# Kernel tuning notes

Hardware: AMD Instinct MI355X
Metric: run time of the kernel (lower is better)

The kernel has to match this reference:

```python
import jax, jax.numpy as jnp
import numpy as np

H, HK, HD = 6, 2, 128  # n_heads, n_kv_heads, head_dim (from AcousticTransformerArgs defaults)


def setup_inputs() -> dict:
    key = jax.random.key(0)
    k1, k2, k3, k4, k5 = jax.random.split(key, 5)
    B, S, D = 2, 4096, 768
    s = 0.02
    return {
        "x": jax.random.normal(k1, (B, S, D), dtype=jnp.float32),
        "wq": jax.random.normal(k2, (H * HD, D), dtype=jnp.float32) * s,
        "wk": jax.random.normal(k3, (HK * HD, D), dtype=jnp.float32) * s,
        "wv": jax.random.normal(k4, (HK * HD, D), dtype=jnp.float32) * s,
        "wo": jax.random.normal(k5, (D, H * HD), dtype=jnp.float32) * s,
    }


def reference(x, wq, wk, wv, wo):
    B, S, D = x.shape
    rep = H // HK  # GQA repeat factor (3)
    scale = 1.0 / jnp.sqrt(jnp.asarray(HD, x.dtype))
    # projections (torch Linear: y = x @ W^T)
    q = (x @ wq.T).reshape(B, S, HK, rep, HD) * scale  # head h = g*rep + r
    k = (x @ wk.T).reshape(B, S, HK, HD)
    v = (x @ wv.T).reshape(B, S, HK, HD)
    # bidirectional (no mask) attention with GQA broadcast instead of physical repeat
    scores = jnp.einsum("bsgrd,btgd->bgrst", q, k)  # [B,HK,rep,S,S]
    attn = jax.nn.softmax(scores, axis=-1)
    out = jnp.einsum("bgrst,btgd->bsgrd", attn, v).reshape(B, S, H * HD)
    return out @ wo.T
```

## Files before the change

### kernel.cpp

```cpp
#include <hip/hip_runtime.h>
#include <hip/hip_bf16.h>
#include <type_traits>

using bf16 = __hip_bfloat16;
typedef __attribute__((ext_vector_type(8))) short bf16x8;
typedef __attribute__((ext_vector_type(4))) float floatx4;

static constexpr int Bb = 2, S = 4096, D = 768, H = 6, HK = 2, HD = 128, REP = 3;
static constexpr int M_ROWS = Bb * S;
static constexpr int NQKV = 1280;

__device__ __forceinline__ floatx4 mfma16(bf16x8 a, bf16x8 b, floatx4 c) {
  return __builtin_amdgcn_mfma_f32_16x16x32_bf16(a, b, c, 0, 0, 0);
}

__device__ __forceinline__ void gld_lds16(const bf16* g, bf16* l) {
  __builtin_amdgcn_global_load_lds(
      (const __attribute__((address_space(1))) unsigned int*)g,
      (__attribute__((address_space(3))) unsigned int*)l, 16, 0, 0);
}

#if defined(__has_builtin)
#if __has_builtin(__builtin_amdgcn_exp2f)
#define EXP2F(x) __builtin_amdgcn_exp2f(x)
#endif
#endif
#ifndef EXP2F
#define EXP2F(x) exp2f(x)
#endif

__device__ __forceinline__ unsigned pk2(float a, float b) {
  unsigned ua = __builtin_bit_cast(unsigned, a) + 0x8000u;
  unsigned ub = __builtin_bit_cast(unsigned, b) + 0x8000u;
#if defined(__has_builtin) && __has_builtin(__builtin_amdgcn_perm)
  return __builtin_amdgcn_perm(ub, ua, 0x07060302);
#else
  return (ua >> 16) | (ub & 0xffff0000u);
#endif
}

__device__ __forceinline__ void perm32swap(unsigned& a, unsigned& b) {
  asm volatile("v_permlane32_swap_b32 %0, %1" : "+v"(a), "+v"(b));
}
__device__ __forceinline__ void perm16swap(unsigned& a, unsigned& b) {
  asm volatile("v_permlane16_swap_b32 %0, %1" : "+v"(a), "+v"(b));
}

static constexpr size_t E_X  = (size_t)M_ROWS * D;
static constexpr size_t E_WQ = E_X + (size_t)H * HD * D;
static constexpr size_t E_WK = E_WQ + (size_t)HK * HD * D;
static constexpr size_t E_WV = E_WK + (size_t)HK * HD * D;
static constexpr size_t E_WO = E_WV + (size_t)D * H * HD;

__global__ __launch_bounds__(256) void cvt_all(const float* __restrict__ x,
                                               const float* __restrict__ wq,
                                               const float* __restrict__ wk,
                                               const float* __restrict__ wv,
                                               const float* __restrict__ wo,
                                               bf16* __restrict__ xb,
                                               bf16* __restrict__ wqkvb,
                                               bf16* __restrict__ wob, float qscale) {
  size_t i = ((size_t)blockIdx.x * 256 + threadIdx.x) * 4;
  const float* src;
  bf16* dst;
  float s = 1.f;
  size_t off;
  if (i < E_X)        { src = x;  dst = xb;                 off = i; }
  else if (i < E_WQ)  { src = wq; dst = wqkvb;              off = i - E_X; s = qscale; }
  else if (i < E_WK)  { src = wk; dst = wqkvb + 589824;     off = i - E_WQ; }
  else if (i < E_WV)  { src = wv; dst = wqkvb + 786432;     off = i - E_WK; }
  else                { src = wo; dst = wob;                off = i - E_WV; }
  float4 v = *(const float4*)(src + off);
  uint2 st;
  st.x = pk2(v.x * s, v.y * s);
  st.y = pk2(v.z * s, v.w * s);
  *(uint2*)(dst + off) = st;
}

template <typename OutT, bool VT_FUSE>
__global__ __launch_bounds__(256, 3) void gemm_bt(const bf16* __restrict__ A,
                                                  const bf16* __restrict__ W,
                                                  OutT* __restrict__ C,
                                                  bf16* __restrict__ Vt,
                                                  int M, int N, int K) {
  const int tid = threadIdx.x;
  const int wave = tid >> 6, lane = tid & 63;
  const int quad = lane >> 4, lq = lane & 15;
  const int m0 = blockIdx.x * 128, n0 = blockIdx.y * 128;
  const int wm = (wave & 1) * 64, wn = (wave >> 1) * 64;

  __shared__ __align__(16) bf16 As[128 * 64];
  __shared__ __align__(16) bf16 Ws[128 * 64];

  floatx4 acc[4][4] = {};

  const int srow = lane >> 3, sc = lane & 7;

  for (int k0 = 0; k0 < K; k0 += 64) {
#pragma unroll
    for (int i = 0; i < 4; ++i) {
      int ig = wave * 4 + i;
      int r = ig * 8 + srow;
      int c = sc ^ (r & 7);
      gld_lds16(&A[(size_t)(m0 + r) * K + k0 + c * 8], &As[ig * 512]);
      gld_lds16(&W[(size_t)(n0 + r) * K + k0 + c * 8], &Ws[ig * 512]);
    }
    __syncthreads();
#pragma unroll
    for (int kh = 0; kh < 2; ++kh) {
      bf16x8 af[4], wf[4];
#pragma unroll
      for (int i = 0; i < 4; ++i) {
        int ra = wm + i * 16 + lq, rw = wn + i * 16 + lq;
        af[i] = *(const bf16x8*)&As[ra * 64 + (((kh * 4 + quad) ^ (ra & 7)) * 8)];
        wf[i] = *(const bf16x8*)&Ws[rw * 64 + (((kh * 4 + quad) ^ (rw & 7)) * 8)];
      }
#pragma unroll
      for (int i = 0; i < 4; ++i)
#pragma unroll
        for (int j = 0; j < 4; ++j) acc[i][j] = mfma16(af[i], wf[j], acc[i][j]);
    }
    __syncthreads();
  }

  if (VT_FUSE && n0 >= 1024) {
    bf16* tb = (wave < 2 ? As : Ws) + (wave & 1) * 4096;
    char* tc = (char*)tb;
#pragma unroll
    for (int i = 0; i < 4; ++i)
#pragma unroll
      for (int j = 0; j < 4; ++j) {
        uint2 st;
        st.x = pk2(acc[i][j][0], acc[i][j][1]);
        st.y = pk2(acc[i][j][2], acc[i][j][3]);
        int col = j * 16 + lq;
        int cc = (i * 2 + (quad >> 1)) ^ (col & 7);
        *(uint2*)(tc + col * 128 + cc * 16 + (quad & 1) * 8) = st;
      }
    const int b = m0 >> 12;
    const int dd_off = lane >> 3, schunk = lane & 7;
    const int sbase = (m0 & 4095) + wm + schunk * 8;
#pragma unroll
    for (int e = 0; e < 8; ++e) {
      int cl = e * 8 + dd_off;
      int col = (n0 - 1024) + wn + cl;
      int gg = col >> 7, dd = col & 127;
      bf16x8 vv = *(const bf16x8*)(tc + cl * 128 + ((schunk ^ (cl & 7)) * 16));
      *(bf16x8*)&Vt[((size_t)(b * HK + gg) * HD + dd) * S + sbase] = vv;
    }
    return;
  }
#pragma unroll
  for (int i = 0; i < 4; ++i)
#pragma unroll
    for (int j = 0; j < 4; ++j)
#pragma unroll
      for (int r = 0; r < 4; ++r) {
        int row = m0 + wm + i * 16 + quad * 4 + r;
        int col = n0 + wn + j * 16 + lq;
        float v = acc[i][j][r];
        if constexpr (std::is_same_v<OutT, float>)
          C[(size_t)row * N + col] = v;
        else
          C[(size_t)row * N + col] = __float2bfloat16(v);
      }
}

__global__ __launch_bounds__(256, 3) void gemm_out(const bf16* __restrict__ A,
                                                   const bf16* __restrict__ W,
                                                   float* __restrict__ C,
                                                   int M, int N, int K) {
  const int tid = threadIdx.x;
  const int wave = tid >> 6, lane = tid & 63;
  const int quad = lane >> 4, lq = lane & 15;
  const int m0 = blockIdx.x * 128, n0 = blockIdx.y * 64;
  const int wm = (wave & 1) * 64, wn = (wave >> 1) * 32;

  __shared__ __align__(16) bf16 As[128 * 64];
  __shared__ __align__(16) bf16 Ws[64 * 64];

  floatx4 acc[4][2] = {};

  const int srow = lane >> 3, sc = lane & 7;

  for (int k0 = 0; k0 < K; k0 += 64) {
#pragma unroll
    for (int i = 0; i < 4; ++i) {
      int ig = wave * 4 + i;
      int r = ig * 8 + srow;
      int c = sc ^ (r & 7);
      gld_lds16(&A[(size_t)(m0 + r) * K + k0 + c * 8], &As[ig * 512]);
    }
#pragma unroll
    for (int i = 0; i < 2; ++i) {
      int ig = wave * 2 + i;
      int r = ig * 8 + srow;
      int c = sc ^ (r & 7);
      gld_lds16(&W[(size_t)(n0 + r) * K + k0 + c * 8], &Ws[ig * 512]);
    }
    __syncthreads();
#pragma unroll
    for (int kh = 0; kh < 2; ++kh) {
      bf16x8 af[4], wf[2];
#pragma unroll
      for (int i = 0; i < 4; ++i) {
        int ra = wm + i * 16 + lq;
        af[i] = *(const bf16x8*)&As[ra * 64 + (((kh * 4 + quad) ^ (ra & 7)) * 8)];
      }
#pragma unroll
      for (int j = 0; j < 2; ++j) {
        int rw = wn + j * 16 + lq;
        wf[j] = *(const bf16x8*)&Ws[rw * 64 + (((kh * 4 + quad) ^ (rw & 7)) * 8)];
      }
#pragma unroll
      for (int i = 0; i < 4; ++i)
#pragma unroll
        for (int j = 0; j < 2; ++j) acc[i][j] = mfma16(af[i], wf[j], acc[i][j]);
    }
    __syncthreads();
  }
#pragma unroll
  for (int i = 0; i < 4; ++i)
#pragma unroll
    for (int j = 0; j < 2; ++j)
#pragma unroll
      for (int r = 0; r < 4; ++r) {
        int row = m0 + wm + i * 16 + quad * 4 + r;
        int col = n0 + wn + j * 16 + lq;
        C[(size_t)row * N + col] = acc[i][j][r];
      }
}

__global__ __launch_bounds__(256, 2) void flash_attn(const bf16* __restrict__ QKV,
                                                     const bf16* __restrict__ Vt,
                                                     bf16* __restrict__ O) {
  const int bid = blockIdx.x;
  const int bg = (bid & 7) >> 1;
  const int b = bg >> 1, g = bg & 1;
  const int qt = ((bid >> 3) << 1) | (bid & 1);
  const int q0 = qt * 32;

  const int tid = threadIdx.x;
  const int w = tid >> 6, lane = tid & 63;
  const int half = w >> 1, wp = w & 1;
  const int quad = lane >> 4, lq = lane & 15;

  __shared__ __align__(16) char smem[81920];
  bf16* Ks = (bf16*)smem;
  bf16* Vs = (bf16*)(smem + 32768);

  const bf16* Kgh = QKV + (size_t)b * S * NQKV + H * HD + g * HD + (size_t)half * 2048 * NQKV;
  const bf16* Vgh = Vt + (size_t)(b * HK + g) * HD * S + half * 2048;

  auto stage = [&](int t0, int kbuf, int vbuf) {
    bf16* kd = Ks + (kbuf * 2 + half) * 4096;
    bf16* vd = Vs + (vbuf * 2 + half) * 4096;
#pragma unroll
    for (int i = 0; i < 4; ++i) {
      int ig = wp * 4 + i;
      int tl = ig * 4 + (lane >> 4);
      int c = (lane & 15) ^ (tl & 15);
      gld_lds16(Kgh + (size_t)(t0 + tl) * NQKV + c * 8, kd + ig * 512);
    }
#pragma unroll
    for (int i = 0; i < 4; ++i) {
      int ig = wp * 4 + i;
      int dl = ig * 16 + (lane >> 2);
      int c = (lane & 3) ^ ((dl >> 1) & 3);
      gld_lds16(Vgh + (size_t)dl * S + t0 + c * 8, vd + ig * 512);
    }
  };

  stage(0, 0, 0);

  const bf16* Qg = QKV + ((size_t)b * S + q0 + wp * 16 + lq) * NQKV + g * REP * HD;
  bf16x8 qf[3][4];
#pragma unroll
  for (int u = 0; u < 3; ++u)
#pragma unroll
    for (int kk = 0; kk < 4; ++kk)
      qf[u][kk] = *(const bf16x8*)(Qg + u * HD + kk * 32 + quad * 8);

  bf16x8 ones;
#pragma unroll
  for (int j = 0; j < 8; ++j) ones[j] = (short)0x3F80;

  floatx4 o[3][8] = {};
  floatx4 lacc[3] = {};
  bf16x8 pf_prev[3];
  const int sw = (lq >> 1) & 3;

#pragma unroll 2
  for (int it = 0; it < 64; ++it) {
    const int kcur = it & 1;
    __syncthreads();
    if (it + 1 < 64) stage((it + 1) * 32, kcur ^ 1, (it + 1) % 3);

    const bf16* ks = Ks + (kcur * 2 + half) * 4096;

    floatx4 sf[3][2] = {};
    __builtin_amdgcn_s_setprio(1);
#pragma unroll
    for (int tt = 0; tt < 2; ++tt)
#pragma unroll
      for (int kk = 0; kk < 4; ++kk) {
        int c = (kk * 4 + quad) ^ lq;
        bf16x8 kf = *(const bf16x8*)&ks[(tt * 16 + lq) * 128 + c * 8];
#pragma unroll
        for (int u = 0; u < 3; ++u) sf[u][tt] = mfma16(kf, qf[u][kk], sf[u][tt]);
      }

    if (it) {
      const bf16* vs = Vs + ((((it - 1) % 3) * 2) + half) * 4096;
#pragma unroll
      for (int u = 0; u < 3; ++u) lacc[u] = mfma16(ones, pf_prev[u], lacc[u]);
#pragma unroll
      for (int dd = 0; dd < 8; ++dd) {
        bf16x8 vf = *(const bf16x8*)&vs[(dd * 16 + lq) * 32 + ((quad ^ sw) * 8)];
#pragma unroll
        for (int u = 0; u < 3; ++u) o[u][dd] = mfma16(vf, pf_prev[u], o[u][dd]);
      }
    }
    __builtin_amdgcn_s_setprio(0);

#pragma unroll
    for (int u = 0; u < 3; ++u) {
      unsigned A0 = pk2(EXP2F(sf[u][0][0]), EXP2F(sf[u][0][1]));
      unsigned A1 = pk2(EXP2F(sf[u][0][2]), EXP2F(sf[u][0][3]));
      unsigned B0 = pk2(EXP2F(sf[u][1][0]), EXP2F(sf[u][1][1]));
      unsigned B1 = pk2(EXP2F(sf[u][1][2]), EXP2F(sf[u][1][3]));
      perm32swap(A0, B0);
      perm16swap(A0, B0);
      perm32swap(A1, B1);
      perm16swap(A1, B1);
      union { unsigned d[4]; bf16x8 v; } pu;
      pu.d[0] = A0; pu.d[1] = A1; pu.d[2] = B0; pu.d[3] = B1;
      pf_prev[u] = pu.v;
    }
  }

  {
    const bf16* vs = Vs + (0 * 2 + half) * 4096;
#pragma unroll
    for (int u = 0; u < 3; ++u) lacc[u] = mfma16(ones, pf_prev[u], lacc[u]);
#pragma unroll
    for (int dd = 0; dd < 8; ++dd) {
      bf16x8 vf = *(const bf16x8*)&vs[(dd * 16 + lq) * 32 + ((quad ^ sw) * 8)];
#pragma unroll
      for (int u = 0; u < 3; ++u) o[u][dd] = mfma16(vf, pf_prev[u], o[u][dd]);
    }
  }

  __syncthreads();
  floatx4* oscr = (floatx4*)smem;
  float* lscr = (float*)(smem + 49152);
  if (half == 1) {
#pragma unroll
    for (int u = 0; u < 3; ++u) {
#pragma unroll
      for (int dd = 0; dd < 8; ++dd)
        oscr[((wp * 3 + u) * 8 + dd) * 64 + lane] = o[u][dd];
      lscr[(wp * 3 + u) * 64 + lane] = lacc[u][0];
    }
  }
  __syncthreads();
  if (half == 0) {
    const size_t row = (size_t)b * S + q0 + wp * 16 + lq;
#pragma unroll
    for (int u = 0; u < 3; ++u) {
      float l = lacc[u][0] + lscr[(wp * 3 + u) * 64 + lane];
      float rinv = 1.0f / l;
#pragma unroll
      for (int dd = 0; dd < 8; ++dd) {
        floatx4 oc = o[u][dd] + oscr[((wp * 3 + u) * 8 + dd) * 64 + lane];
        uint2 st;
        st.x = pk2(oc[0] * rinv, oc[1] * rinv);
        st.y = pk2(oc[2] * rinv, oc[3] * rinv);
        int col = (g * REP + u) * HD + dd * 16 + quad * 4;
        *(uint2*)&O[row * (H * HD) + col] = st;
      }
    }
  }
}

static inline size_t al256(size_t x) { return (x + 255) & ~size_t(255); }

extern "C" void kernel_launch(void* const* d_in, const int* in_sizes, int n_in,
                              void* d_out, int out_size, void* d_ws, size_t ws_size,
                              hipStream_t stream) {
  const float* x  = (const float*)d_in[0];
  const float* wq = (const float*)d_in[1];
  const float* wk = (const float*)d_in[2];
  const float* wv = (const float*)d_in[3];
  const float* wo = (const float*)d_in[4];
  float* out = (float*)d_out;

  char* w = (char*)d_ws;
  size_t off = 0;
  auto carve = [&](size_t elems) {
    bf16* p = (bf16*)(w + off);
    off = al256(off + elems * sizeof(bf16));
    return p;
  };
  bf16* xb    = carve((size_t)M_ROWS * D);
  bf16* wqkvb = carve((size_t)NQKV * D);
  bf16* wob   = carve((size_t)D * (H * HD));
  bf16* QKVb  = carve((size_t)M_ROWS * NQKV);
  bf16* Vtb   = carve((size_t)M_ROWS * (HK * HD));
  bf16* Ab    = carve((size_t)M_ROWS * (H * HD));

  const float qscale = 0.1275174465f;

  cvt_all<<<(int)(E_WO / 1024), 256, 0, stream>>>(x, wq, wk, wv, wo, xb, wqkvb, wob, qscale);

  gemm_bt<bf16, true><<<dim3(M_ROWS / 128, NQKV / 128), 256, 0, stream>>>(
      xb, wqkvb, QKVb, Vtb, M_ROWS, NQKV, D);

  flash_attn<<<512, 256, 0, stream>>>(QKVb, Vtb, Ab);

  gemm_out<<<dim3(M_ROWS / 128, D / 64), 256, 0, stream>>>(
      Ab, wob, out, M_ROWS, D, H * HD);
}
```

Baseline: 220.9 us.

## Remove split-KV halves in flash attention; two waves scan full sequence

Flash attention blocks drop from four waves (two KV halves) to two waves that each iterate over the full key sequence. This removes the shared-memory cross-half reduction and its barriers, halves shared memory per block, and precomputes staging pointers incremented each step. In exchange, each block runs twice as many serial iterations with fewer waves, reducing latency hiding.

```diff
diff --git a/kernel.cpp b/kernel.cpp
--- a/kernel.cpp
+++ b/kernel.cpp
@@ -231,7 +231,7 @@
       }
 }
 
-__global__ __launch_bounds__(256, 2) void flash_attn(const bf16* __restrict__ QKV,
+__global__ __launch_bounds__(128, 2) void flash_attn(const bf16* __restrict__ QKV,
                                                      const bf16* __restrict__ Vt,
                                                      bf16* __restrict__ O) {
   const int bid = blockIdx.x;
@@ -241,37 +241,43 @@
   const int q0 = qt * 32;
 
   const int tid = threadIdx.x;
-  const int w = tid >> 6, lane = tid & 63;
-  const int half = w >> 1, wp = w & 1;
+  const int wp = tid >> 6, lane = tid & 63;
   const int quad = lane >> 4, lq = lane & 15;
 
-  __shared__ __align__(16) char smem[81920];
+  __shared__ __align__(16) char smem[40960];
   bf16* Ks = (bf16*)smem;
-  bf16* Vs = (bf16*)(smem + 32768);
-
-  const bf16* Kgh = QKV + (size_t)b * S * NQKV + H * HD + g * HD + (size_t)half * 2048 * NQKV;
-  const bf16* Vgh = Vt + (size_t)(b * HK + g) * HD * S + half * 2048;
-
-  auto stage = [&](int t0, int kbuf, int vbuf) {
-    bf16* kd = Ks + (kbuf * 2 + half) * 4096;
-    bf16* vd = Vs + (vbuf * 2 + half) * 4096;
-#pragma unroll
-    for (int i = 0; i < 4; ++i) {
-      int ig = wp * 4 + i;
-      int tl = ig * 4 + (lane >> 4);
-      int c = (lane & 15) ^ (tl & 15);
-      gld_lds16(Kgh + (size_t)(t0 + tl) * NQKV + c * 8, kd + ig * 512);
-    }
-#pragma unroll
-    for (int i = 0; i < 4; ++i) {
-      int ig = wp * 4 + i;
-      int dl = ig * 16 + (lane >> 2);
-      int c = (lane & 3) ^ ((dl >> 1) & 3);
-      gld_lds16(Vgh + (size_t)dl * S + t0 + c * 8, vd + ig * 512);
-    }
+  bf16* Vs = (bf16*)(smem + 16384);
+
+  const bf16* Kgh = QKV + (size_t)b * S * NQKV + H * HD + g * HD;
+  const bf16* Vgh = Vt + (size_t)(b * HK + g) * HD * S;
+
+  const bf16* kp[4];
+  const bf16* vp[4];
+#pragma unroll
+  for (int i = 0; i < 4; ++i) {
+    int tl = wp * 16 + i * 4 + (lane >> 4);
+    int c = (lane & 15) ^ (tl & 15);
+    kp[i] = Kgh + (size_t)tl * NQKV + c * 8;
+  }
+#pragma unroll
+  for (int i = 0; i < 4; ++i) {
+    int dl = wp * 64 + i * 16 + (lane >> 2);
+    int c = (lane & 3) ^ ((dl >> 1) & 3);
+    vp[i] = Vgh + (size_t)dl * S + c * 8;
+  }
+
+  auto stage = [&](int kbuf, int vbuf) {
+    bf16* kd = Ks + kbuf * 4096;
+    bf16* vd = Vs + vbuf * 4096;
+#pragma unroll
+    for (int i = 0; i < 4; ++i) gld_lds16(kp[i], kd + (wp * 4 + i) * 512);
+#pragma unroll
+    for (int i = 0; i < 4; ++i) gld_lds16(vp[i], vd + (wp * 4 + i) * 512);
+#pragma unroll
+    for (int i = 0; i < 4; ++i) { kp[i] += 32 * NQKV; vp[i] += 32; }
   };
 
-  stage(0, 0, 0);
+  stage(0, 0);
 
   const bf16* Qg = QKV + ((size_t)b * S + q0 + wp * 16 + lq) * NQKV + g * REP * HD;
   bf16x8 qf[3][4];
@@ -291,12 +297,11 @@
   const int sw = (lq >> 1) & 3;
 
 #pragma unroll 2
-  for (int it = 0; it < 64; ++it) {
-    const int kcur = it & 1;
+  for (int it = 0; it < 128; ++it) {
     __syncthreads();
-    if (it + 1 < 64) stage((it + 1) * 32, kcur ^ 1, (it + 1) % 3);
-
-    const bf16* ks = Ks + (kcur * 2 + half) * 4096;
+    if (it + 1 < 128) stage((it + 1) & 1, (it + 1) % 3);
+
+    const bf16* ks = Ks + (it & 1) * 4096;
 
     floatx4 sf[3][2] = {};
     __builtin_amdgcn_s_setprio(1);
@@ -311,7 +316,7 @@
       }
 
     if (it) {
-      const bf16* vs = Vs + ((((it - 1) % 3) * 2) + half) * 4096;
+      const bf16* vs = Vs + ((it - 1) % 3) * 4096;
 #pragma unroll
       for (int u = 0; u < 3; ++u) lacc[u] = mfma16(ones, pf_prev[u], lacc[u]);
 #pragma unroll
@@ -340,7 +345,7 @@
   }
 
   {
-    const bf16* vs = Vs + (0 * 2 + half) * 4096;
+    const bf16* vs = Vs + 1 * 4096;
 #pragma unroll
     for (int u = 0; u < 3; ++u) lacc[u] = mfma16(ones, pf_prev[u], lacc[u]);
 #pragma unroll
@@ -351,34 +356,17 @@
     }
   }
 
-  __syncthreads();
-  floatx4* oscr = (floatx4*)smem;
-  float* lscr = (float*)(smem + 49152);
-  if (half == 1) {
-#pragma unroll
-    for (int u = 0; u < 3; ++u) {
-#pragma unroll
-      for (int dd = 0; dd < 8; ++dd)
-        oscr[((wp * 3 + u) * 8 + dd) * 64 + lane] = o[u][dd];
-      lscr[(wp * 3 + u) * 64 + lane] = lacc[u][0];
-    }
-  }
-  __syncthreads();
-  if (half == 0) {
-    const size_t row = (size_t)b * S + q0 + wp * 16 + lq;
-#pragma unroll
-    for (int u = 0; u < 3; ++u) {
-      float l = lacc[u][0] + lscr[(wp * 3 + u) * 64 + lane];
-      float rinv = 1.0f / l;
-#pragma unroll
-      for (int dd = 0; dd < 8; ++dd) {
-        floatx4 oc = o[u][dd] + oscr[((wp * 3 + u) * 8 + dd) * 64 + lane];
-        uint2 st;
-        st.x = pk2(oc[0] * rinv, oc[1] * rinv);
-        st.y = pk2(oc[2] * rinv, oc[3] * rinv);
-        int col = (g * REP + u) * HD + dd * 16 + quad * 4;
-        *(uint2*)&O[row * (H * HD) + col] = st;
-      }
+  const size_t row = (size_t)b * S + q0 + wp * 16 + lq;
+#pragma unroll
+  for (int u = 0; u < 3; ++u) {
+    float rinv = 1.0f / lacc[u][0];
+#pragma unroll
+    for (int dd = 0; dd < 8; ++dd) {
+      uint2 st;
+      st.x = pk2(o[u][dd][0] * rinv, o[u][dd][1] * rinv);
+      st.y = pk2(o[u][dd][2] * rinv, o[u][dd][3] * rinv);
+      int col = (g * REP + u) * HD + dd * 16 + quad * 4;
+      *(uint2*)&O[row * (H * HD) + col] = st;
     }
   }
 }
@@ -416,7 +404,7 @@
   gemm_bt<bf16, true><<<dim3(M_ROWS / 128, NQKV / 128), 256, 0, stream>>>(
       xb, wqkvb, QKVb, Vtb, M_ROWS, NQKV, D);
 
-  flash_attn<<<512, 256, 0, stream>>>(QKVb, Vtb, Ab);
+  flash_attn<<<512, 128, 0, stream>>>(QKVb, Vtb, Ab);
 
   gemm_out<<<dim3(M_ROWS / 128, D / 64), 256, 0, stream>>>(
       Ab, wob, out, M_ROWS, D, H * HD);
```

After: 267.3 us. +21.0%, slower.
